# Performance work log

Hardware: AMD Instinct MI355X
Metric: run time of the kernel (lower is better)

Reference implementation:

```python
import jax, jax.numpy as jnp
import numpy as np

N_BINS = 15


def setup_inputs() -> dict:
    key = jax.random.key(0)
    k1, k2 = jax.random.split(key)
    N, C = 500000, 100
    logits = jax.random.normal(k1, (N, C), dtype=jnp.float32)
    labels = jax.random.randint(k2, (N,), 0, C, dtype=jnp.int64)
    return {"logits": logits, "labels": labels}


def _classwise_ece(logits, labels, n_bins=N_BINS):
    # Fused equivalent of the per-class, per-bin double loop.
    # Bins are (lower, upper] with boundaries linspace(0,1,n_bins+1),
    # so bin index = ceil(p * n_bins) - 1; p == 0 falls in NO bin.
    probs = jax.nn.softmax(logits, axis=1)            # [N, C]
    N, C = probs.shape
    valid = probs > 0.0                               # p==0 matched by no (lower, upper] bin
    bin_idx = jnp.clip(jnp.ceil(probs * n_bins).astype(jnp.int32) - 1, 0, n_bins - 1)

    class_ids = jnp.arange(C, dtype=jnp.int32)[None, :]          # [1, C]
    key = (jnp.broadcast_to(class_ids * n_bins, probs.shape) + bin_idx).reshape(-1)  # [N*C]

    w = valid.astype(probs.dtype)
    correct = (labels[:, None] == class_ids).astype(probs.dtype)  # labels_in_class

    num_seg = C * n_bins
    count = jax.ops.segment_sum(w.reshape(-1), key, num_segments=num_seg).reshape(C, n_bins)
    conf_sum = jax.ops.segment_sum((probs * w).reshape(-1), key, num_segments=num_seg).reshape(C, n_bins)
    acc_sum = jax.ops.segment_sum((correct * w).reshape(-1), key, num_segments=num_seg).reshape(C, n_bins)

    # |avg_conf - acc| * prop_in_bin == |conf_sum - acc_sum| / N; empty bins give 0.
    per_class_sce = jnp.sum(jnp.abs(conf_sum - acc_sum), axis=1) / N   # [C]
    sce = jnp.mean(per_class_sce)
    return sce, per_class_sce


def reference(logits, labels):
    return _classwise_ece(logits, labels)
```

## Files before the change

### kernel.cpp

```cpp
#include <hip/hip_runtime.h>
#include <math.h>

#define NCLS 100
#define NBINS 15
#define NSEG (NCLS * NBINS)
#define NTOT (2 * NSEG + NCLS)
#define PSTRIDE 3104
#define RPI 8
#define GMAIN 1536
#define SWEEP (GMAIN * 4 * RPI)

__device__ __forceinline__ void fadd(float* p, float v) { unsafeAtomicAdd(p, v); }

__device__ __forceinline__ float readlane_f(float x, int l) {
    return __builtin_bit_cast(float, __builtin_amdgcn_readlane(__builtin_bit_cast(int, x), l));
}

template <int CTRL>
__device__ __forceinline__ float dpp_add(float x) {
    int y = __builtin_amdgcn_update_dpp(0, __builtin_bit_cast(int, x),
                                        CTRL, 0xf, 0xf, true);
    return x + __builtin_bit_cast(float, y);
}


#define LOAD_TILE(E0, E1, E2, E3, LAB, TB) do {                               \
    (LAB) = labels[min((TB) + lane, N - 1)];                                  \
    const int _f = ((TB) + h) * NCLS + cqc;                                   \
    (E0) = *(const float4*)(logits + min(_f,            flim));               \
    (E1) = *(const float4*)(logits + min(_f + 2 * NCLS, flim));               \
    (E2) = *(const float4*)(logits + min(_f + 4 * NCLS, flim));               \
    (E3) = *(const float4*)(logits + min(_f + 6 * NCLS, flim));               \
} while (0)

#define EXPMASK(E, SOUT, VM) do {                                             \
    float _ex = __expf((E).x), _ey = __expf((E).y);                           \
    float _ez = __expf((E).z), _ew = __expf((E).w);                           \
    (E).x = (VM) ? _ex : 0.f; (E).y = (VM) ? _ey : 0.f;                       \
    (E).z = (VM) ? _ez : 0.f; (E).w = (VM) ? _ew : 0.f;                       \
    SOUT = ((E).x + (E).y) + ((E).z + (E).w);                                 \
} while (0)

#define CLS_TAIL(EV, J, INV, LABV) do {                                       \
    const float _p = (EV) * (INV);                                            \
    t##J += _p;                                                               \
    const float _pf = _p * 15.f;                                              \
    const bool _ch = _pf > 1.0f;                                              \
    const bool _lh = (cq + (J)) == (LABV);                                    \
    if (_ch || _lh) {                                                         \
        const int _b = min((int)ceilf(_pf) - 1, NBINS - 1);                   \
        if (_ch) fadd(&s_conf[(cq + (J)) * NBINS + _b], _p);                  \
        if (_lh) fadd(&s_acc[(cq + (J)) * NBINS + max(_b, 0)], 1.f);          \
    }                                                                         \
} while (0)

#define SLOT_TAIL(E, K, SV, TB, LAB, FULLV) do {                              \
    const float _te = readlane_f(SV, 31);                                     \
    const float _to = readlane_f(SV, 63);                                     \
    const float _inv = __builtin_amdgcn_rcpf(fmaxf(h ? _to : _te, 1e-30f));   \
    int _le = __builtin_amdgcn_readlane(LAB, 2 * (K));                        \
    int _lo = __builtin_amdgcn_readlane(LAB, 2 * (K) + 1);                    \
    if (!(FULLV)) {                                                           \
        if ((TB) + 2 * (K)     >= N) _le = -1;                                \
        if ((TB) + 2 * (K) + 1 >= N) _lo = -1;                                \
    }                                                                         \
    const int _lab = h ? _lo : _le;                                           \
    CLS_TAIL((E).x, 0, _inv, _lab);                                           \
    CLS_TAIL((E).y, 1, _inv, _lab);                                           \
    CLS_TAIL((E).z, 2, _inv, _lab);                                           \
    CLS_TAIL((E).w, 3, _inv, _lab);                                           \
} while (0)

#define COMPUTE_TILE(E0, E1, E2, E3, LAB, TB, FULLV) do {                     \
    const bool _v0 = act && ((FULLV) || ((TB) + 0 + h) < N);                  \
    const bool _v1 = act && ((FULLV) || ((TB) + 2 + h) < N);                  \
    const bool _v2 = act && ((FULLV) || ((TB) + 4 + h) < N);                  \
    const bool _v3 = act && ((FULLV) || ((TB) + 6 + h) < N);                  \
    float _s0, _s1, _s2, _s3;                                                 \
    EXPMASK(E0, _s0, _v0); EXPMASK(E1, _s1, _v1);                             \
    EXPMASK(E2, _s2, _v2); EXPMASK(E3, _s3, _v3);                             \
    _s0 = dpp_add<0x111>(_s0); _s1 = dpp_add<0x111>(_s1);                     \
    _s2 = dpp_add<0x111>(_s2); _s3 = dpp_add<0x111>(_s3);                     \
    _s0 = dpp_add<0x112>(_s0); _s1 = dpp_add<0x112>(_s1);                     \
    _s2 = dpp_add<0x112>(_s2); _s3 = dpp_add<0x112>(_s3);                     \
    _s0 = dpp_add<0x114>(_s0); _s1 = dpp_add<0x114>(_s1);                     \
    _s2 = dpp_add<0x114>(_s2); _s3 = dpp_add<0x114>(_s3);                     \
    _s0 = dpp_add<0x118>(_s0); _s1 = dpp_add<0x118>(_s1);                     \
    _s2 = dpp_add<0x118>(_s2); _s3 = dpp_add<0x118>(_s3);                     \
    _s0 = dpp_add<0x142>(_s0); _s1 = dpp_add<0x142>(_s1);                     \
    _s2 = dpp_add<0x142>(_s2); _s3 = dpp_add<0x142>(_s3);                     \
    SLOT_TAIL(E0, 0, _s0, TB, LAB, FULLV);                                    \
    SLOT_TAIL(E1, 1, _s1, TB, LAB, FULLV);                                    \
    SLOT_TAIL(E2, 2, _s2, TB, LAB, FULLV);                                    \
    SLOT_TAIL(E3, 3, _s3, TB, LAB, FULLV);                                    \
} while (0)

__global__ __launch_bounds__(256, 6) void ece_main_kernel(
    const float* __restrict__ logits,
    const int* __restrict__ labels,
    float* __restrict__ g_hist,
    float* __restrict__ parts,
    int N)
{
    __shared__ float s_conf[NSEG];
    __shared__ float s_acc[NSEG];
    __shared__ float s_total[NCLS];
    for (int i = threadIdx.x; i < NSEG; i += 256) { s_conf[i] = 0.f; s_acc[i] = 0.f; }
    if (threadIdx.x < NCLS) s_total[threadIdx.x] = 0.f;
    __syncthreads();

    const int lane  = threadIdx.x & 63;
    const int wave  = threadIdx.x >> 6;
    const int gwave = blockIdx.x * 4 + wave;
    const int q     = lane & 31;
    const int h     = lane >> 5;
    const int cq    = 4 * q;
    const int cqc   = min(cq, NCLS - 4);
    const bool act  = (q < NCLS / 4);
    const int flim  = N * NCLS - 4;

    float t0 = 0.f, t1 = 0.f, t2 = 0.f, t3 = 0.f;
    float4 A0, A1, A2, A3, B0, B1, B2, B3;
    int labA, labB;
    int base = gwave * RPI;

    LOAD_TILE(A0, A1, A2, A3, labA, base);
    while (base + SWEEP + RPI <= N) {
        LOAD_TILE(B0, B1, B2, B3, labB, base + SWEEP);
        __builtin_amdgcn_sched_barrier(0);
        COMPUTE_TILE(A0, A1, A2, A3, labA, base, true);
        LOAD_TILE(A0, A1, A2, A3, labA, base + 2 * SWEEP);
        __builtin_amdgcn_sched_barrier(0);
        COMPUTE_TILE(B0, B1, B2, B3, labB, base + SWEEP, true);
        base += 2 * SWEEP;
    }
    if (base < N) COMPUTE_TILE(A0, A1, A2, A3, labA, base, false);
    if (base + SWEEP < N) {
        LOAD_TILE(B0, B1, B2, B3, labB, base + SWEEP);
        COMPUTE_TILE(B0, B1, B2, B3, labB, base + SWEEP, false);
    }

    if (act) {
        fadd(&s_total[cq + 0], t0);
        fadd(&s_total[cq + 1], t1);
        fadd(&s_total[cq + 2], t2);
        fadd(&s_total[cq + 3], t3);
    }
    __syncthreads();

    if (parts) {
        float* my = parts + (size_t)blockIdx.x * PSTRIDE;
        for (int i = threadIdx.x; i < NSEG; i += 256) {
            my[i] = s_conf[i];
            my[NSEG + i] = s_acc[i];
        }
        if (threadIdx.x < NCLS)
            my[2 * NSEG + threadIdx.x] = s_total[threadIdx.x];
    } else {
        for (int i = threadIdx.x; i < NSEG; i += 256) {
            float v = s_conf[i]; if (v != 0.f) fadd(&g_hist[i], v);
            float a = s_acc[i];  if (a != 0.f) fadd(&g_hist[NSEG + i], a);
        }
        if (threadIdx.x < NCLS) {
            float tt = s_total[threadIdx.x];
            if (tt != 0.f) fadd(&g_hist[2 * NSEG + threadIdx.x], tt);
        }
    }
}

__global__ __launch_bounds__(1024) void ece_reduce_kernel(
    const float* __restrict__ parts, float* __restrict__ g_hist, int nparts)
{
    const int lane = threadIdx.x & 63;
    const int wave = threadIdx.x >> 6;
    const int cell = blockIdx.x * 64 + lane;
    const int per = nparts / 16;
    float s = 0.f;
    if (cell < NTOT) {
        const float* bp = parts + (size_t)wave * per * PSTRIDE + cell;
        #pragma unroll 8
        for (int p = 0; p < per; ++p)
            s += bp[(size_t)p * PSTRIDE];
    }
    __shared__ float red[16][64];
    red[wave][lane] = s;
    __syncthreads();
    if (wave == 0) {
        float v = 0.f;
        #pragma unroll
        for (int w = 0; w < 16; ++w) v += red[w][lane];
        if (cell < NTOT) g_hist[cell] = v;
    }
}

__global__ __launch_bounds__(128) void ece_final_kernel(
    const float* __restrict__ g_hist,
    float* __restrict__ out,
    float invN)
{
    __shared__ float red[128];
    const int t = threadIdx.x;
    float s = 0.f;
    if (t < NCLS) {
        float conf0 = g_hist[2 * NSEG + t];
        float sum = 0.f;
        #pragma unroll
        for (int b = 1; b < NBINS; ++b) {
            float cb = g_hist[t * NBINS + b];
            float ab = g_hist[NSEG + t * NBINS + b];
            conf0 -= cb;
            sum += fabsf(cb - ab);
        }
        sum += fabsf(conf0 - g_hist[NSEG + t * NBINS + 0]);
        s = sum * invN;
        out[1 + t] = s;
    }
    red[t] = s;
    __syncthreads();
    #pragma unroll
    for (int off = 64; off > 0; off >>= 1) {
        if (t < off) red[t] += red[t + off];
        __syncthreads();
    }
    if (t == 0) out[0] = red[0] * (1.0f / (float)NCLS);
}

extern "C" void kernel_launch(void* const* d_in, const int* in_sizes, int n_in,
                              void* d_out, int out_size, void* d_ws, size_t ws_size,
                              hipStream_t stream)
{
    const float* logits = (const float*)d_in[0];
    const int*   labels = (const int*)d_in[1];
    const int N = in_sizes[1];
    float* out = (float*)d_out;

    float* g_hist = (float*)d_ws;
    const size_t parts_off = ((size_t)NTOT * sizeof(float) + 255) & ~(size_t)255;
    const size_t need = parts_off + (size_t)GMAIN * PSTRIDE * sizeof(float);
    float* parts = (ws_size >= need) ? (float*)((char*)d_ws + parts_off) : nullptr;

    if (!parts)
        (void)hipMemsetAsync(d_ws, 0, (size_t)NTOT * sizeof(float), stream);

    ece_main_kernel<<<GMAIN, 256, 0, stream>>>(logits, labels, g_hist, parts, N);
    if (parts)
        ece_reduce_kernel<<<(NTOT + 63) / 64, 1024, 0, stream>>>(parts, g_hist, GMAIN);
    ece_final_kernel<<<1, 128, 0, stream>>>(g_hist, out, 1.0f / (float)N);
}
```

Before: 296.2 us.

## Assign contiguous row ranges per wave, raise occupancy, defer probability multiply

Each wave now processes one contiguous chunk of rows instead of grid-strided tiles, with the grid grown to 2048 blocks and launch bounds raised to 8 blocks per CU. The bin-threshold test now compares the raw exponential against sum/15, so the normalized probability is only computed when an atomic is needed, and the class total is accumulated with an fma. Contiguous chunks should give each wave a sequential stream of memory, and higher occupancy should hide more latency. The cost is that neighboring waves no longer touch adjacent addresses at the same time, and the tighter register budget may cause spills.

```diff
diff --git a/kernel.cpp b/kernel.cpp
--- a/kernel.cpp
+++ b/kernel.cpp
@@ -7,8 +7,8 @@
 #define NTOT (2 * NSEG + NCLS)
 #define PSTRIDE 3104
 #define RPI 8
-#define GMAIN 1536
-#define SWEEP (GMAIN * 4 * RPI)
+#define GMAIN 2048
+#define NWAVES (GMAIN * 4)
 
 __device__ __forceinline__ void fadd(float* p, float v) { unsafeAtomicAdd(p, v); }
 
@@ -41,41 +41,42 @@
     SOUT = ((E).x + (E).y) + ((E).z + (E).w);                                 \
 } while (0)
 
-#define CLS_TAIL(EV, J, INV, LABV) do {                                       \
-    const float _p = (EV) * (INV);                                            \
-    t##J += _p;                                                               \
-    const float _pf = _p * 15.f;                                              \
-    const bool _ch = _pf > 1.0f;                                              \
+#define CLS_TAIL(EV, J, INV, TH, LABV) do {                                   \
+    t##J = fmaf((EV), (INV), t##J);                                           \
+    const bool _ch = (EV) > (TH);                                             \
     const bool _lh = (cq + (J)) == (LABV);                                    \
     if (_ch || _lh) {                                                         \
-        const int _b = min((int)ceilf(_pf) - 1, NBINS - 1);                   \
+        const float _p = (EV) * (INV);                                        \
+        const int _b = min((int)ceilf(_p * 15.f) - 1, NBINS - 1);             \
         if (_ch) fadd(&s_conf[(cq + (J)) * NBINS + _b], _p);                  \
         if (_lh) fadd(&s_acc[(cq + (J)) * NBINS + max(_b, 0)], 1.f);          \
     }                                                                         \
 } while (0)
 
-#define SLOT_TAIL(E, K, SV, TB, LAB, FULLV) do {                              \
+#define SLOT_TAIL(E, K, SV, TB, LAB, FULLV, REND) do {                        \
     const float _te = readlane_f(SV, 31);                                     \
     const float _to = readlane_f(SV, 63);                                     \
-    const float _inv = __builtin_amdgcn_rcpf(fmaxf(h ? _to : _te, 1e-30f));   \
+    const float _S  = h ? _to : _te;                                          \
+    const float _inv = __builtin_amdgcn_rcpf(fmaxf(_S, 1e-30f));              \
+    const float _th  = _S * (1.0f / 15.0f);                                   \
     int _le = __builtin_amdgcn_readlane(LAB, 2 * (K));                        \
     int _lo = __builtin_amdgcn_readlane(LAB, 2 * (K) + 1);                    \
     if (!(FULLV)) {                                                           \
-        if ((TB) + 2 * (K)     >= N) _le = -1;                                \
-        if ((TB) + 2 * (K) + 1 >= N) _lo = -1;                                \
+        if ((TB) + 2 * (K)     >= (REND)) _le = -1;                           \
+        if ((TB) + 2 * (K) + 1 >= (REND)) _lo = -1;                           \
     }                                                                         \
     const int _lab = h ? _lo : _le;                                           \
-    CLS_TAIL((E).x, 0, _inv, _lab);                                           \
-    CLS_TAIL((E).y, 1, _inv, _lab);                                           \
-    CLS_TAIL((E).z, 2, _inv, _lab);                                           \
-    CLS_TAIL((E).w, 3, _inv, _lab);                                           \
-} while (0)
-
-#define COMPUTE_TILE(E0, E1, E2, E3, LAB, TB, FULLV) do {                     \
-    const bool _v0 = act && ((FULLV) || ((TB) + 0 + h) < N);                  \
-    const bool _v1 = act && ((FULLV) || ((TB) + 2 + h) < N);                  \
-    const bool _v2 = act && ((FULLV) || ((TB) + 4 + h) < N);                  \
-    const bool _v3 = act && ((FULLV) || ((TB) + 6 + h) < N);                  \
+    CLS_TAIL((E).x, 0, _inv, _th, _lab);                                      \
+    CLS_TAIL((E).y, 1, _inv, _th, _lab);                                      \
+    CLS_TAIL((E).z, 2, _inv, _th, _lab);                                      \
+    CLS_TAIL((E).w, 3, _inv, _th, _lab);                                      \
+} while (0)
+
+#define COMPUTE_TILE(E0, E1, E2, E3, LAB, TB, FULLV, REND) do {               \
+    const bool _v0 = act && ((FULLV) || ((TB) + 0 + h) < (REND));             \
+    const bool _v1 = act && ((FULLV) || ((TB) + 2 + h) < (REND));             \
+    const bool _v2 = act && ((FULLV) || ((TB) + 4 + h) < (REND));             \
+    const bool _v3 = act && ((FULLV) || ((TB) + 6 + h) < (REND));             \
     float _s0, _s1, _s2, _s3;                                                 \
     EXPMASK(E0, _s0, _v0); EXPMASK(E1, _s1, _v1);                             \
     EXPMASK(E2, _s2, _v2); EXPMASK(E3, _s3, _v3);                             \
@@ -89,13 +90,13 @@
     _s2 = dpp_add<0x118>(_s2); _s3 = dpp_add<0x118>(_s3);                     \
     _s0 = dpp_add<0x142>(_s0); _s1 = dpp_add<0x142>(_s1);                     \
     _s2 = dpp_add<0x142>(_s2); _s3 = dpp_add<0x142>(_s3);                     \
-    SLOT_TAIL(E0, 0, _s0, TB, LAB, FULLV);                                    \
-    SLOT_TAIL(E1, 1, _s1, TB, LAB, FULLV);                                    \
-    SLOT_TAIL(E2, 2, _s2, TB, LAB, FULLV);                                    \
-    SLOT_TAIL(E3, 3, _s3, TB, LAB, FULLV);                                    \
-} while (0)
-
-__global__ __launch_bounds__(256, 6) void ece_main_kernel(
+    SLOT_TAIL(E0, 0, _s0, TB, LAB, FULLV, REND);                              \
+    SLOT_TAIL(E1, 1, _s1, TB, LAB, FULLV, REND);                              \
+    SLOT_TAIL(E2, 2, _s2, TB, LAB, FULLV, REND);                              \
+    SLOT_TAIL(E3, 3, _s3, TB, LAB, FULLV, REND);                              \
+} while (0)
+
+__global__ __launch_bounds__(256, 8) void ece_main_kernel(
     const float* __restrict__ logits,
     const int* __restrict__ labels,
     float* __restrict__ g_hist,
@@ -119,25 +120,31 @@
     const bool act  = (q < NCLS / 4);
     const int flim  = N * NCLS - 4;
 
+    const int per  = N / NWAVES;
+    const int rem  = N - per * NWAVES;
+    const int r0   = gwave * per + min(gwave, rem);
+    const int rend = r0 + per + (gwave < rem ? 1 : 0);
+
     float t0 = 0.f, t1 = 0.f, t2 = 0.f, t3 = 0.f;
     float4 A0, A1, A2, A3, B0, B1, B2, B3;
     int labA, labB;
-    int base = gwave * RPI;
+    int base = r0;
 
     LOAD_TILE(A0, A1, A2, A3, labA, base);
-    while (base + SWEEP + RPI <= N) {
-        LOAD_TILE(B0, B1, B2, B3, labB, base + SWEEP);
+    while (base + 2 * RPI <= rend) {
+        LOAD_TILE(B0, B1, B2, B3, labB, base + RPI);
         __builtin_amdgcn_sched_barrier(0);
-        COMPUTE_TILE(A0, A1, A2, A3, labA, base, true);
-        LOAD_TILE(A0, A1, A2, A3, labA, base + 2 * SWEEP);
+        COMPUTE_TILE(A0, A1, A2, A3, labA, base, true, rend);
+        LOAD_TILE(A0, A1, A2, A3, labA, base + 2 * RPI);
         __builtin_amdgcn_sched_barrier(0);
-        COMPUTE_TILE(B0, B1, B2, B3, labB, base + SWEEP, true);
-        base += 2 * SWEEP;
-    }
-    if (base < N) COMPUTE_TILE(A0, A1, A2, A3, labA, base, false);
-    if (base + SWEEP < N) {
-        LOAD_TILE(B0, B1, B2, B3, labB, base + SWEEP);
-        COMPUTE_TILE(B0, B1, B2, B3, labB, base + SWEEP, false);
+        COMPUTE_TILE(B0, B1, B2, B3, labB, base + RPI, true, rend);
+        base += 2 * RPI;
+    }
+    if (base < rend)
+        COMPUTE_TILE(A0, A1, A2, A3, labA, base, false, rend);
+    if (base + RPI < rend) {
+        LOAD_TILE(B0, B1, B2, B3, labB, base + RPI);
+        COMPUTE_TILE(B0, B1, B2, B3, labB, base + RPI, false, rend);
     }
 
     if (act) {
```

Result: slower. 347.9 us (+17.5%).
